# Performance work log

Measured on AMD Instinct MI355X. Metric: run time of the kernel, lower is better.

The kernel has to match this reference:

```python
import jax, jax.numpy as jnp
import numpy as np

SQ, B, NP, HN = 2048, 2, 16, 64  # [seq, batch, heads, head_dim]

def setup_inputs() -> dict:
    key = jax.random.key(0)
    kq, kk, kv = jax.random.split(key, 3)
    return {
        "query": jax.random.normal(kq, (SQ, B, NP, HN), dtype=jnp.float32),
        "key":   jax.random.normal(kk, (SQ, B, NP, HN), dtype=jnp.float32),
        "value": jax.random.normal(kv, (SQ, B, NP, HN), dtype=jnp.float32),
    }

def reference(query, key, value):
    sq, b, nheads, hn = query.shape
    # NOTE: original module computes norm_factor=sqrt(hn) but never applies it;
    # scores are UNscaled QK^T, replicated faithfully here.
    scores = jnp.einsum('sbnh,tbnh->bnst', query, key)          # [b, np, sq, sk]
    probs = jax.nn.softmax(scores, axis=-1)                      # mask=None -> plain softmax
    # dropout is deterministic (train=False default) -> identity
    context = jnp.einsum('bnst,tbnh->sbnh', probs, value)        # [sq, b, np, hn]
    return context.reshape(sq, b, nheads * hn).astype(jnp.float32)
```

## Files before the change

### kernel.cpp

```cpp
#include <hip/hip_runtime.h>
#include <math.h>
#include <stdint.h>

#define SQ 2048
#define NBH 32
#define HN 64
#define BQ 128
#define BK2 128
#define NP2 (SQ/BK2)
#define TOK 2048
#define HSTRIDE (SQ*HN)

typedef _Float16 half2v __attribute__((ext_vector_type(2)));
typedef _Float16 half4v __attribute__((ext_vector_type(4)));
typedef _Float16 half8v __attribute__((ext_vector_type(8)));
typedef float f32x16 __attribute__((ext_vector_type(16)));

__device__ __forceinline__ void async16(const void* g, void* l) {
  __builtin_amdgcn_global_load_lds(
      (const __attribute__((address_space(1))) void*)g,
      (__attribute__((address_space(3))) void*)l, 16, 0, 0);
}

__device__ __forceinline__ float fexp2(float x) {
#if __has_builtin(__builtin_amdgcn_exp2f)
  return __builtin_amdgcn_exp2f(x);
#else
  return exp2f(x);
#endif
}

__device__ __forceinline__ float xmax32(float x) {
#if __has_builtin(__builtin_amdgcn_permlane32_swap)
  auto r = __builtin_amdgcn_permlane32_swap(__float_as_int(x), __float_as_int(x),
                                            false, false);
  return fmaxf(__int_as_float(r[0]), __int_as_float(r[1]));
#else
  return fmaxf(x, __shfl_xor(x, 32, 64));
#endif
}
__device__ __forceinline__ float xadd32(float x) {
#if __has_builtin(__builtin_amdgcn_permlane32_swap)
  auto r = __builtin_amdgcn_permlane32_swap(__float_as_int(x), __float_as_int(x),
                                            false, false);
  return __int_as_float(r[0]) + __int_as_float(r[1]);
#else
  return x + __shfl_xor(x, 32, 64);
#endif
}

__global__ __launch_bounds__(256) void prep_kv(const float* __restrict__ K,
                                               const float* __restrict__ V,
                                               _Float16* __restrict__ Kh,
                                               _Float16* __restrict__ Vt) {
  __shared__ _Float16 vs[HN * 64];
  const int t = threadIdx.x;
  const int head = blockIdx.y;
  {
    const int key = blockIdx.x * 64 + (t >> 2);
    const int c0 = (t & 3) * 2;
    const float* src = K + (size_t)key * TOK + head * HN + c0 * 8;
    float4 a = *(const float4*)src;
    float4 b = *(const float4*)(src + 4);
    float4 c = *(const float4*)(src + 8);
    float4 d = *(const float4*)(src + 12);
    half8v h0, h1;
    h0[0]=(_Float16)a.x; h0[1]=(_Float16)a.y; h0[2]=(_Float16)a.z; h0[3]=(_Float16)a.w;
    h0[4]=(_Float16)b.x; h0[5]=(_Float16)b.y; h0[6]=(_Float16)b.z; h0[7]=(_Float16)b.w;
    h1[0]=(_Float16)c.x; h1[1]=(_Float16)c.y; h1[2]=(_Float16)c.z; h1[3]=(_Float16)c.w;
    h1[4]=(_Float16)d.x; h1[5]=(_Float16)d.y; h1[6]=(_Float16)d.z; h1[7]=(_Float16)d.w;
    _Float16* row = Kh + (size_t)head * HSTRIDE + (size_t)key * 64;
    *(half8v*)&row[((c0    ) ^ (key & 7)) * 8] = h0;
    *(half8v*)&row[((c0 + 1) ^ (key & 7)) * 8] = h1;
  }
  {
    const int kt = blockIdx.x * 64;
    const int kl = (t >> 3) * 2;
    const int db = (t & 7) * 8;
    const float* src = V + (size_t)(kt + kl) * TOK + head * HN + db;
    float4 a0 = *(const float4*)src;
    float4 a1 = *(const float4*)(src + 4);
    float4 b0 = *(const float4*)(src + TOK);
    float4 b1 = *(const float4*)(src + TOK + 4);
    const float av[8] = {a0.x,a0.y,a0.z,a0.w,a1.x,a1.y,a1.z,a1.w};
    const float bv[8] = {b0.x,b0.y,b0.z,b0.w,b1.x,b1.y,b1.z,b1.w};
    const int u = kl >> 2;
    #pragma unroll
    for (int j = 0; j < 8; ++j) {
      const int dim = db + j;
      const int pos = u ^ (dim & 15);
      half2v h; h[0] = (_Float16)av[j]; h[1] = (_Float16)bv[j];
      *(half2v*)&vs[dim * 64 + pos * 4 + (kl & 3)] = h;
    }
    __syncthreads();
    const int dim = t >> 2;
    const int q = (t & 3) ^ (dim & 3);
    const _Float16* srow = &vs[dim * 64 + q * 16];
    _Float16* drow = Vt + (size_t)head * HSTRIDE + (size_t)dim * SQ + kt + q * 16;
    *(half8v*)&drow[0] = *(const half8v*)&srow[0];
    *(half8v*)&drow[8] = *(const half8v*)&srow[8];
  }
}

__global__ __launch_bounds__(512, 4)
void fattn_mfma(const float* __restrict__ Q, const _Float16* __restrict__ Kh,
                const _Float16* __restrict__ Vt, float* __restrict__ O) {
  __shared__ __align__(16) _Float16 smem[4 * 8192];
  _Float16* kbf = smem;
  _Float16* vtf = smem + 16384;

  const int t = threadIdx.x;
  const int lane = t & 63;
  const int w = t >> 6;
  const int qw = w & 3;
  const int g = w >> 2;
  const int h2 = lane >> 5;
  const int l31 = lane & 31;
  const int q0 = blockIdx.x * BQ + qw * 32;
  const int head = blockIdx.y;
  const _Float16* Kp = Kh + (size_t)head * HSTRIDE;
  const _Float16* Vp = Vt + (size_t)head * HSTRIDE;
  const int tb = g * 4096;

  half8v qf[4];
  {
    const float* qp = Q + (size_t)(q0 + l31) * TOK + head * HN + 8 * h2;
    const float s = 1.44269504088896f;
    #pragma unroll
    for (int ks = 0; ks < 4; ++ks) {
      float4 a = *(const float4*)(qp + 16 * ks);
      float4 b = *(const float4*)(qp + 16 * ks + 4);
      half8v f;
      f[0] = (_Float16)(s*a.x); f[1] = (_Float16)(s*a.y); f[2] = (_Float16)(s*a.z); f[3] = (_Float16)(s*a.w);
      f[4] = (_Float16)(s*b.x); f[5] = (_Float16)(s*b.y); f[6] = (_Float16)(s*b.z); f[7] = (_Float16)(s*b.w);
      qf[ks] = f;
    }
  }

  f32x16 acc0, acc1;
  #pragma unroll
  for (int r = 0; r < 16; ++r) { acc0[r] = 0.f; acc1[r] = 0.f; }
  float m_i = -INFINITY, l_i = 0.f;

  auto stage = [&](int p) {
    const int buf = p & 1;
    const size_t kt = (size_t)p * BK2;
    #pragma unroll
    for (int i = 0; i < 2; ++i) {
      const int off = w * 512 + i * 4096;
      async16(Kp + kt * 64 + off + lane * 8, kbf + buf * 8192 + off);
    }
    #pragma unroll
    for (int tl = 0; tl < 2; ++tl) {
      const int off = w * 512;
      const int eo = off + lane * 8;
      const int dim = eo >> 6, inner = eo & 63;
      async16(Vp + (size_t)dim * SQ + kt + tl * 64 + inner,
              vtf + buf * 8192 + tl * 4096 + off);
    }
  };

  stage(0);
  for (int p = 0; p < NP2; ++p) {
    __syncthreads();
    if (p + 1 < NP2) stage(p + 1);
    const int cur = p & 1;
    const _Float16* kb = kbf + cur * 8192 + tb;
    const _Float16* vb = vtf + cur * 8192 + tb;

    f32x16 c0, c1;
    #pragma unroll
    for (int r = 0; r < 16; ++r) { c0[r] = 0.f; c1[r] = 0.f; }
    #pragma unroll
    for (int ks = 0; ks < 4; ++ks) {
      const int pos = ((h2 + 2 * ks) ^ (l31 & 7)) * 8;
      half8v a0v = *(const half8v*)&kb[l31 * 64 + pos];
      half8v a1v = *(const half8v*)&kb[(l31 + 32) * 64 + pos];
      c0 = __builtin_amdgcn_mfma_f32_32x32x16_f16(a0v, qf[ks], c0, 0, 0, 0);
      c1 = __builtin_amdgcn_mfma_f32_32x32x16_f16(a1v, qf[ks], c1, 0, 0, 0);
    }

    float mx0 = fmaxf(c0[0], c1[0]);
    float mx1 = fmaxf(c0[1], c1[1]);
    float mx2 = fmaxf(c0[2], c1[2]);
    float mx3 = fmaxf(c0[3], c1[3]);
    #pragma unroll
    for (int r = 4; r < 16; r += 4) {
      mx0 = fmaxf(mx0, fmaxf(c0[r],     c1[r]));
      mx1 = fmaxf(mx1, fmaxf(c0[r + 1], c1[r + 1]));
      mx2 = fmaxf(mx2, fmaxf(c0[r + 2], c1[r + 2]));
      mx3 = fmaxf(mx3, fmaxf(c0[r + 3], c1[r + 3]));
    }
    float mx = fmaxf(fmaxf(mx0, mx1), fmaxf(mx2, mx3));
    mx = xmax32(mx);
    const float mnew = fmaxf(m_i, mx);
    const float alpha = fexp2(m_i - mnew);
    float rs0 = 0.f, rs1 = 0.f;
    #pragma unroll
    for (int r = 0; r < 16; ++r) {
      float p0 = fexp2(c0[r] - mnew);
      float p1 = fexp2(c1[r] - mnew);
      c0[r] = p0; c1[r] = p1;
      rs0 += p0; rs1 += p1;
    }
    float rsum = xadd32(rs0 + rs1);
    l_i = l_i * alpha + rsum;
    m_i = mnew;
    #pragma unroll
    for (int r = 0; r < 16; ++r) { acc0[r] *= alpha; acc1[r] *= alpha; }

    #pragma unroll
    for (int ks = 0; ks < 4; ++ks) {
      const int rb = 8 * (ks & 1);
      const f32x16& s = (ks < 2) ? c0 : c1;
      union { half8v v8; half2v v2[4]; } pu;
      #pragma unroll
      for (int tt = 0; tt < 4; ++tt) {
        auto pk = __builtin_amdgcn_cvt_pkrtz(s[rb + 2 * tt], s[rb + 2 * tt + 1]);
        pu.v2[tt] = *(half2v*)&pk;
      }
      #pragma unroll
      for (int mbd = 0; mbd < 2; ++mbd) {
        const int dim = l31 + 32 * mbd;
        const int sw = dim & 15;
        union { half8v v8; half4v v4[2]; } au;
        au.v4[0] = *(const half4v*)&vb[dim * 64 + ((4 * ks + h2)     ^ sw) * 4];
        au.v4[1] = *(const half4v*)&vb[dim * 64 + ((4 * ks + 2 + h2) ^ sw) * 4];
        if (mbd == 0)
          acc0 = __builtin_amdgcn_mfma_f32_32x32x16_f16(au.v8, pu.v8, acc0, 0, 0, 0);
        else
          acc1 = __builtin_amdgcn_mfma_f32_32x32x16_f16(au.v8, pu.v8, acc1, 0, 0, 0);
      }
    }
  }

  __syncthreads();
  float* fb = (float*)smem;
  const int slot = qw * 64 + lane;
  if (g == 1) {
    #pragma unroll
    for (int r = 0; r < 16; ++r) {
      fb[slot * 32 + r]      = acc0[r];
      fb[slot * 32 + 16 + r] = acc1[r];
    }
    fb[8192 + slot] = m_i;
    fb[8448 + slot] = l_i;
  }
  __syncthreads();
  if (g == 0) {
    const float m2 = fb[8192 + slot];
    const float l2 = fb[8448 + slot];
    const float ms = fmaxf(m_i, m2);
    const float a0 = fexp2(m_i - ms);
    const float a1 = fexp2(m2 - ms);
    const float invl = 1.f / (l_i * a0 + l2 * a1);
    float* orow = O + (size_t)(q0 + l31) * TOK + head * HN;
    #pragma unroll
    for (int r = 0; r < 16; ++r) {
      const int d = (r & 3) + 8 * (r >> 2) + 4 * h2;
      orow[d]      = (acc0[r] * a0 + fb[slot * 32 + r]      * a1) * invl;
      orow[d + 32] = (acc1[r] * a0 + fb[slot * 32 + 16 + r] * a1) * invl;
    }
  }
}

extern "C" void kernel_launch(void* const* d_in, const int* in_sizes, int n_in,
                              void* d_out, int out_size, void* d_ws, size_t ws_size,
                              hipStream_t stream) {
  const float* Q = (const float*)d_in[0];
  const float* K = (const float*)d_in[1];
  const float* V = (const float*)d_in[2];
  float* O = (float*)d_out;
  _Float16* Kh = (_Float16*)d_ws;
  _Float16* Vh = Kh + (size_t)NBH * HSTRIDE;
  prep_kv<<<dim3(SQ / 64, NBH), 256, 0, stream>>>(K, V, Kh, Vh);
  fattn_mfma<<<dim3(SQ / BQ, NBH), 512, 0, stream>>>(Q, Kh, Vh, O);
}
```

Before: 143.0 us.

## Load K/V fragments directly from global into registers, drop LDS staging

Replaces the double-buffered async global-to-LDS staging of K and V tiles with direct per-lane global loads into registers, using the pre-swizzled workspace layout. Block size shrinks to 256 threads and 64 queries per block, and the two key-split groups each walk half the sequence independently with no per-tile barriers. It also adds s_setprio around the MFMA sections. This removes LDS traffic and the barriers between tiles, but each block no longer shares K/V tiles through LDS, so global and L2 traffic goes up and load latency is exposed without explicit prefetch.

```diff
diff --git a/kernel.cpp b/kernel.cpp
--- a/kernel.cpp
+++ b/kernel.cpp
@@ -5,9 +5,6 @@
 #define SQ 2048
 #define NBH 32
 #define HN 64
-#define BQ 128
-#define BK2 128
-#define NP2 (SQ/BK2)
 #define TOK 2048
 #define HSTRIDE (SQ*HN)
 
@@ -15,12 +12,6 @@
 typedef _Float16 half4v __attribute__((ext_vector_type(4)));
 typedef _Float16 half8v __attribute__((ext_vector_type(8)));
 typedef float f32x16 __attribute__((ext_vector_type(16)));
-
-__device__ __forceinline__ void async16(const void* g, void* l) {
-  __builtin_amdgcn_global_load_lds(
-      (const __attribute__((address_space(1))) void*)g,
-      (__attribute__((address_space(3))) void*)l, 16, 0, 0);
-}
 
 __device__ __forceinline__ float fexp2(float x) {
 #if __has_builtin(__builtin_amdgcn_exp2f)
@@ -102,25 +93,27 @@
   }
 }
 
-__global__ __launch_bounds__(512, 4)
+__global__ __launch_bounds__(256, 2)
 void fattn_mfma(const float* __restrict__ Q, const _Float16* __restrict__ Kh,
                 const _Float16* __restrict__ Vt, float* __restrict__ O) {
-  __shared__ __align__(16) _Float16 smem[4 * 8192];
-  _Float16* kbf = smem;
-  _Float16* vtf = smem + 16384;
+  __shared__ __align__(16) float fb[128 * 32 + 256];
 
   const int t = threadIdx.x;
   const int lane = t & 63;
   const int w = t >> 6;
-  const int qw = w & 3;
-  const int g = w >> 2;
+  const int qw = w & 1;
+  const int g = w >> 1;
   const int h2 = lane >> 5;
   const int l31 = lane & 31;
-  const int q0 = blockIdx.x * BQ + qw * 32;
+  const int sw7 = l31 & 7;
+  const int sw15 = l31 & 15;
+  const int q0 = blockIdx.x * 64 + qw * 32;
   const int head = blockIdx.y;
-  const _Float16* Kp = Kh + (size_t)head * HSTRIDE;
-  const _Float16* Vp = Vt + (size_t)head * HSTRIDE;
-  const int tb = g * 4096;
+
+  const _Float16* kRow0 = Kh + (size_t)head * HSTRIDE + (size_t)(g * 1024 + l31) * 64;
+  const _Float16* kRow1 = kRow0 + 32 * 64;
+  const _Float16* vRow0 = Vt + (size_t)head * HSTRIDE + (size_t)l31 * SQ + g * 1024;
+  const _Float16* vRow1 = vRow0 + (size_t)32 * SQ;
 
   half8v qf[4];
   {
@@ -142,43 +135,36 @@
   for (int r = 0; r < 16; ++r) { acc0[r] = 0.f; acc1[r] = 0.f; }
   float m_i = -INFINITY, l_i = 0.f;
 
-  auto stage = [&](int p) {
-    const int buf = p & 1;
-    const size_t kt = (size_t)p * BK2;
-    #pragma unroll
-    for (int i = 0; i < 2; ++i) {
-      const int off = w * 512 + i * 4096;
-      async16(Kp + kt * 64 + off + lane * 8, kbf + buf * 8192 + off);
-    }
-    #pragma unroll
-    for (int tl = 0; tl < 2; ++tl) {
-      const int off = w * 512;
-      const int eo = off + lane * 8;
-      const int dim = eo >> 6, inner = eo & 63;
-      async16(Vp + (size_t)dim * SQ + kt + tl * 64 + inner,
-              vtf + buf * 8192 + tl * 4096 + off);
-    }
-  };
-
-  stage(0);
-  for (int p = 0; p < NP2; ++p) {
-    __syncthreads();
-    if (p + 1 < NP2) stage(p + 1);
-    const int cur = p & 1;
-    const _Float16* kb = kbf + cur * 8192 + tb;
-    const _Float16* vb = vtf + cur * 8192 + tb;
+  for (int i = 0; i < 16; ++i) {
+    const _Float16* k0t = kRow0 + i * 4096;
+    const _Float16* k1t = kRow1 + i * 4096;
+    const _Float16* v0t = vRow0 + i * 64;
+    const _Float16* v1t = vRow1 + i * 64;
+
+    half4v vf[16];
+    #pragma unroll
+    for (int ks = 0; ks < 4; ++ks) {
+      const int u0 = ((4 * ks + h2)     ^ sw15) * 4;
+      const int u1 = ((4 * ks + 2 + h2) ^ sw15) * 4;
+      vf[ks * 4 + 0] = *(const half4v*)&v0t[u0];
+      vf[ks * 4 + 1] = *(const half4v*)&v0t[u1];
+      vf[ks * 4 + 2] = *(const half4v*)&v1t[u0];
+      vf[ks * 4 + 3] = *(const half4v*)&v1t[u1];
+    }
 
     f32x16 c0, c1;
     #pragma unroll
     for (int r = 0; r < 16; ++r) { c0[r] = 0.f; c1[r] = 0.f; }
-    #pragma unroll
-    for (int ks = 0; ks < 4; ++ks) {
-      const int pos = ((h2 + 2 * ks) ^ (l31 & 7)) * 8;
-      half8v a0v = *(const half8v*)&kb[l31 * 64 + pos];
-      half8v a1v = *(const half8v*)&kb[(l31 + 32) * 64 + pos];
+    __builtin_amdgcn_s_setprio(1);
+    #pragma unroll
+    for (int ks = 0; ks < 4; ++ks) {
+      const int pos = ((2 * ks + h2) ^ sw7) * 8;
+      half8v a0v = *(const half8v*)&k0t[pos];
+      half8v a1v = *(const half8v*)&k1t[pos];
       c0 = __builtin_amdgcn_mfma_f32_32x32x16_f16(a0v, qf[ks], c0, 0, 0, 0);
       c1 = __builtin_amdgcn_mfma_f32_32x32x16_f16(a1v, qf[ks], c1, 0, 0, 0);
     }
+    __builtin_amdgcn_s_setprio(0);
 
     float mx0 = fmaxf(c0[0], c1[0]);
     float mx1 = fmaxf(c0[1], c1[1]);
@@ -191,8 +177,7 @@
       mx2 = fmaxf(mx2, fmaxf(c0[r + 2], c1[r + 2]));
       mx3 = fmaxf(mx3, fmaxf(c0[r + 3], c1[r + 3]));
     }
-    float mx = fmaxf(fmaxf(mx0, mx1), fmaxf(mx2, mx3));
-    mx = xmax32(mx);
+    float mx = xmax32(fmaxf(fmaxf(mx0, mx1), fmaxf(mx2, mx3)));
     const float mnew = fmaxf(m_i, mx);
     const float alpha = fexp2(m_i - mnew);
     float rs0 = 0.f, rs1 = 0.f;
@@ -203,12 +188,12 @@
       c0[r] = p0; c1[r] = p1;
       rs0 += p0; rs1 += p1;
     }
-    float rsum = xadd32(rs0 + rs1);
-    l_i = l_i * alpha + rsum;
+    l_i = l_i * alpha + xadd32(rs0 + rs1);
     m_i = mnew;
     #pragma unroll
     for (int r = 0; r < 16; ++r) { acc0[r] *= alpha; acc1[r] *= alpha; }
 
+    __builtin_amdgcn_s_setprio(1);
     #pragma unroll
     for (int ks = 0; ks < 4; ++ks) {
       const int rb = 8 * (ks & 1);
@@ -221,35 +206,33 @@
       }
       #pragma unroll
       for (int mbd = 0; mbd < 2; ++mbd) {
-        const int dim = l31 + 32 * mbd;
-        const int sw = dim & 15;
         union { half8v v8; half4v v4[2]; } au;
-        au.v4[0] = *(const half4v*)&vb[dim * 64 + ((4 * ks + h2)     ^ sw) * 4];
-        au.v4[1] = *(const half4v*)&vb[dim * 64 + ((4 * ks + 2 + h2) ^ sw) * 4];
+        au.v4[0] = vf[ks * 4 + mbd * 2];
+        au.v4[1] = vf[ks * 4 + mbd * 2 + 1];
         if (mbd == 0)
           acc0 = __builtin_amdgcn_mfma_f32_32x32x16_f16(au.v8, pu.v8, acc0, 0, 0, 0);
         else
           acc1 = __builtin_amdgcn_mfma_f32_32x32x16_f16(au.v8, pu.v8, acc1, 0, 0, 0);
       }
     }
-  }
-
+    __builtin_amdgcn_s_setprio(0);
+  }
+
+  const int slot = qw * 64 + lane;
   __syncthreads();
-  float* fb = (float*)smem;
-  const int slot = qw * 64 + lane;
   if (g == 1) {
     #pragma unroll
     for (int r = 0; r < 16; ++r) {
       fb[slot * 32 + r]      = acc0[r];
       fb[slot * 32 + 16 + r] = acc1[r];
     }
-    fb[8192 + slot] = m_i;
-    fb[8448 + slot] = l_i;
+    fb[4096 + slot] = m_i;
+    fb[4224 + slot] = l_i;
   }
   __syncthreads();
   if (g == 0) {
-    const float m2 = fb[8192 + slot];
-    const float l2 = fb[8448 + slot];
+    const float m2 = fb[4096 + slot];
+    const float l2 = fb[4224 + slot];
     const float ms = fmaxf(m_i, m2);
     const float a0 = fexp2(m_i - ms);
     const float a1 = fexp2(m2 - ms);
@@ -274,5 +257,5 @@
   _Float16* Kh = (_Float16*)d_ws;
   _Float16* Vh = Kh + (size_t)NBH * HSTRIDE;
   prep_kv<<<dim3(SQ / 64, NBH), 256, 0, stream>>>(K, V, Kh, Vh);
-  fattn_mfma<<<dim3(SQ / BQ, NBH), 512, 0, stream>>>(Q, Kh, Vh, O);
-}
+  fattn_mfma<<<dim3(SQ / 64, NBH), 256, 0, stream>>>(Q, Kh, Vh, O);
+}
```

After: 217.8 us. +52.3%, slower.
